# Kernel optimization log

Measured on AMD Instinct MI355X. Metric: run time of the kernel, lower is better.

## Reference

```python
import jax, jax.numpy as jnp
import numpy as np

E = 4_000_000   # number of edges
F = 16          # number of edge features
N = 100_000     # number of nodes (> F, so indices.max()+1 == N in the torch code)


def setup_inputs() -> dict:
    key = jax.random.key(0)
    k1, k2 = jax.random.split(key)
    edge_attrs = jax.random.normal(k1, (E, F), dtype=jnp.float32)
    attr_idx = jax.random.randint(k2, (2, E), 0, N, dtype=jnp.int64)
    # Pin the max node id so torch's data-dependent output size (indices.max()+1)
    # equals N deterministically.
    attr_idx = attr_idx.at[0, 0].set(N - 1)
    return {"edge_attrs": edge_attrs, "attr_idx": attr_idx, "n_nodes": N}


def reference(edge_attrs, attr_idx, n_nodes):
    # Faithful to the torch module: values are edge_attrs.view(-1) in row-major
    # order (e*F + f), but the COO indices are built in tiled order (f*E + e).
    # Hence the value summed into bucket (src[e], feature k) is
    # edge_attrs.flatten()[k*E + e]  ==  edge_attrs.reshape(-1).reshape(F, E)[k, e].
    n_edges, n_feats = edge_attrs.shape
    vals = edge_attrs.reshape(-1).reshape(n_feats, n_edges)  # (F, E)
    src = attr_idx[0]  # parent node per edge; torch.sparse.sum reduces over dst
    out = jax.ops.segment_sum(vals.T, src, num_segments=n_nodes)  # (N, F)
    return out
```

## Files before the change

### kernel.cpp

```cpp
#include <hip/hip_runtime.h>
#include <hip/hip_bf16.h>


#define F_FEATS 16
#define NPB 128
#define NB_MAX 1024
#define EPB 4096
#define TP 1024
#define RPT 4
#define TB 512
#define MAXBLK 1024
#define CAP_MAX 6144
#define RRT (CAP_MAX / TB)

__global__ __launch_bounds__(256) void mp_hist(
    const int* __restrict__ src, int* __restrict__ counts,
    int E, int nbuckets)
{
    __shared__ int s_hist[NB_MAX];
    const int tid = threadIdx.x;
    const int base = blockIdx.x * EPB;
    for (int i = tid; i < nbuckets; i += 256) s_hist[i] = 0;
    __syncthreads();
#pragma unroll
    for (int i = 0; i < 4; ++i) {
        int e = base + tid * 4 + i * 1024;
        if (e + 3 < E) {
            int4 s = *reinterpret_cast<const int4*>(src + e);
            atomicAdd(&s_hist[s.x >> 7], 1);
            atomicAdd(&s_hist[s.y >> 7], 1);
            atomicAdd(&s_hist[s.z >> 7], 1);
            atomicAdd(&s_hist[s.w >> 7], 1);
        } else {
            for (int j = 0; j < 4; ++j)
                if (e + j < E) atomicAdd(&s_hist[src[e + j] >> 7], 1);
        }
    }
    __syncthreads();
    size_t row = (size_t)blockIdx.x * nbuckets;
    for (int i = tid; i < nbuckets; i += 256) counts[row + i] = s_hist[i];
}

__global__ __launch_bounds__(256) void mp_scan(
    int* __restrict__ cnt_bases,
    int* __restrict__ totals, int nblocksA, int nbuckets)
{
    __shared__ int s[MAXBLK];
    const int b = blockIdx.x, tid = threadIdx.x;
    int orig[MAXBLK / 256];
#pragma unroll
    for (int k = 0; k < MAXBLK / 256; ++k) {
        int j = tid + k * 256;
        orig[k] = (j < nblocksA) ? cnt_bases[(size_t)j * nbuckets + b] : 0;
        s[j] = orig[k];
    }
    __syncthreads();
    for (int off = 1; off < MAXBLK; off <<= 1) {
        int v[MAXBLK / 256];
#pragma unroll
        for (int k = 0; k < MAXBLK / 256; ++k) {
            int j = tid + k * 256;
            v[k] = (j >= off) ? s[j - off] : 0;
        }
        __syncthreads();
#pragma unroll
        for (int k = 0; k < MAXBLK / 256; ++k) s[tid + k * 256] += v[k];
        __syncthreads();
    }
#pragma unroll
    for (int k = 0; k < MAXBLK / 256; ++k) {
        int j = tid + k * 256;
        if (j < nblocksA)
            cnt_bases[(size_t)j * nbuckets + b] = s[j] - orig[k];
    }
    if (tid == 0) totals[b] = s[MAXBLK - 1];
}

__global__ __launch_bounds__(TP) void mp_place_sorted(
    const float* __restrict__ vals,
    const int*   __restrict__ src,
    const int*   __restrict__ bases,
    int*         __restrict__ ids,
    float*       __restrict__ vrec,
    int E, int cap, int nbuckets)
{
    __shared__ int s_cnt[NB_MAX];
    __shared__ int s_pre[NB_MAX];
    __shared__ int s_gb[NB_MAX];
    __shared__ int s_pk[EPB];
    __shared__ int s_slot[EPB];
    __shared__ int s_tot;

    const int tid = threadIdx.x;
    const int bs  = blockIdx.x * EPB;
    const int* brow = bases + (size_t)blockIdx.x * nbuckets;

    for (int i = tid; i < NB_MAX; i += TP) s_cnt[i] = 0;
    for (int i = tid; i < nbuckets; i += TP) s_gb[i] = brow[i];
    __syncthreads();

    int n_reg[RPT];
#pragma unroll
    for (int i = 0; i < RPT; ++i) {
        int e = bs + tid + i * TP;
        n_reg[i] = (e < E) ? src[e] : -1;
    }
#pragma unroll
    for (int i = 0; i < RPT; ++i)
        if (n_reg[i] >= 0) atomicAdd(&s_cnt[n_reg[i] >> 7], 1);
    __syncthreads();

    int oc = s_cnt[tid];
    s_pre[tid] = oc;
    __syncthreads();
    for (int off = 1; off < NB_MAX; off <<= 1) {
        int v = (tid >= off) ? s_pre[tid - off] : 0;
        __syncthreads();
        s_pre[tid] += v;
        __syncthreads();
    }
    if (tid == NB_MAX - 1) s_tot = s_pre[tid];
    s_pre[tid] -= oc;
    __syncthreads();
    s_cnt[tid] = s_pre[tid];
    __syncthreads();

#pragma unroll
    for (int i = 0; i < RPT; ++i) {
        int n = n_reg[i];
        if (n < 0) continue;
        int e = bs + tid + i * TP;
        int b = n >> 7;
        int p = atomicAdd(&s_cnt[b], 1);
        s_pk[p] = (n << 12) | (e - bs);
        int r = p - s_pre[b];
        int g = s_gb[b] + r;
        s_slot[p] = (g < cap) ? (b * cap + g) : -1;
    }
    __syncthreads();

    const int total = s_tot;
    int off_r[RPT], slot_r[RPT], pk_r[RPT];
    bool val_r[RPT];
#pragma unroll
    for (int i = 0; i < RPT; ++i) {
        int p = tid + i * TP;
        val_r[i] = (p < total);
        pk_r[i]  = val_r[i] ? s_pk[p] : 0;
        slot_r[i] = val_r[i] ? s_slot[p] : -1;
        off_r[i] = pk_r[i] & 0xFFF;
    }

    float v[RPT][F_FEATS];
#pragma unroll
    for (int k = 0; k < F_FEATS; ++k) {
        const float* row = vals + (size_t)k * E + bs;
#pragma unroll
        for (int i = 0; i < RPT; ++i)
            if (val_r[i]) v[i][k] = row[off_r[i]];
    }

#pragma unroll
    for (int i = 0; i < RPT; ++i) {
        int slot = slot_r[i];
        if (slot >= 0) {
            ids[slot] = pk_r[i] >> 12;
            float4* d = reinterpret_cast<float4*>(vrec + (size_t)slot * F_FEATS);
            d[0] = make_float4(v[i][0],  v[i][1],  v[i][2],  v[i][3]);
            d[1] = make_float4(v[i][4],  v[i][5],  v[i][6],  v[i][7]);
            d[2] = make_float4(v[i][8],  v[i][9],  v[i][10], v[i][11]);
            d[3] = make_float4(v[i][12], v[i][13], v[i][14], v[i][15]);
        }
    }
}

__global__ __launch_bounds__(TB) void mp_reduce_seg(
    const int*   __restrict__ totals,
    const int*   __restrict__ ids,
    const float* __restrict__ vrec,
    float*       __restrict__ out,
    int cap, int N)
{
    __shared__ unsigned short s_perm[CAP_MAX];
    __shared__ int s_cnt[NPB];
    __shared__ int s_start[NPB + 1];
    const int b = blockIdx.x, tid = threadIdx.x;

    for (int i = tid; i < NPB; i += TB) s_cnt[i] = 0;
    __syncthreads();

    int cnt = totals[b];
    if (cnt > cap) cnt = cap;
    const size_t bkt = (size_t)b * cap;
    const int* idr = ids + bkt;

    int loc_r[RRT], rnk_r[RRT];
#pragma unroll
    for (int i = 0; i < RRT; ++i) {
        int r = tid + i * TB;
        if (r < cnt) {
            int l = idr[r] & (NPB - 1);
            loc_r[i] = l;
            rnk_r[i] = atomicAdd(&s_cnt[l], 1);
        } else {
            loc_r[i] = -1; rnk_r[i] = 0;
        }
    }
    __syncthreads();

    if (tid < NPB) s_start[tid + 1] = s_cnt[tid];
    if (tid == 0) s_start[0] = 0;
    __syncthreads();
    for (int off = 1; off < NPB; off <<= 1) {
        int v = 0;
        if (tid < NPB) {
            int j = tid + 1;
            v = (j > off) ? s_start[j - off] : 0;
        }
        __syncthreads();
        if (tid < NPB) s_start[tid + 1] += v;
        __syncthreads();
    }

#pragma unroll
    for (int i = 0; i < RRT; ++i) {
        if (loc_r[i] >= 0)
            s_perm[s_start[loc_r[i]] + rnk_r[i]] = (unsigned short)(tid + i * TB);
    }
    __syncthreads();

    const int g = tid >> 2, q = tid & 3;
    const float4* vr4 = reinterpret_cast<const float4*>(vrec) + bkt * 4;
    int j = s_start[g];
    const int j1 = s_start[g + 1];
    float4 acc = make_float4(0.f, 0.f, 0.f, 0.f);
    for (; j + 1 < j1; j += 2) {
        int r0 = s_perm[j], r1 = s_perm[j + 1];
        float4 v0 = vr4[r0 * 4 + q];
        float4 v1 = vr4[r1 * 4 + q];
        acc.x += v0.x; acc.y += v0.y; acc.z += v0.z; acc.w += v0.w;
        acc.x += v1.x; acc.y += v1.y; acc.z += v1.z; acc.w += v1.w;
    }
    if (j < j1) {
        int r0 = s_perm[j];
        float4 v0 = vr4[r0 * 4 + q];
        acc.x += v0.x; acc.y += v0.y; acc.z += v0.z; acc.w += v0.w;
    }

    int node = b * NPB + g;
    if (node < N)
        reinterpret_cast<float4*>(out)[(size_t)node * 4 + q] = acc;
}

__global__ __launch_bounds__(256) void mp_scatter_fallback(
    const float* __restrict__ vals, const int* __restrict__ src,
    float* __restrict__ out, long long E)
{
    long long e = ((long long)blockIdx.x * blockDim.x + threadIdx.x) * 4;
    if (e >= E) return;
    int4 s = *reinterpret_cast<const int4*>(src + e);
    long long b0 = (long long)s.x * F_FEATS, b1 = (long long)s.y * F_FEATS;
    long long b2 = (long long)s.z * F_FEATS, b3 = (long long)s.w * F_FEATS;
#pragma unroll
    for (int k = 0; k < F_FEATS; ++k) {
        float4 v = *reinterpret_cast<const float4*>(vals + (long long)k * E + e);
        atomicAdd(out + b0 + k, v.x);
        atomicAdd(out + b1 + k, v.y);
        atomicAdd(out + b2 + k, v.z);
        atomicAdd(out + b3 + k, v.w);
    }
}

extern "C" void kernel_launch(void* const* d_in, const int* in_sizes, int n_in,
                              void* d_out, int out_size, void* d_ws, size_t ws_size,
                              hipStream_t stream) {
    const float* edge_attrs = (const float*)d_in[0];
    const int*   attr_idx   = (const int*)d_in[1];
    int E = in_sizes[1] / 2;
    int N = out_size / F_FEATS;

    int nbuckets = (N + NPB - 1) / NPB;
    int gridA    = (E + EPB - 1) / EPB;
    long long avg = (long long)E / nbuckets;
    int cap = (int)(((avg + avg / 8 + 255) / 256) * 256);

    size_t off_tot    = 0;
    size_t off_counts = ((size_t)nbuckets * 4 + 255) & ~(size_t)255;
    size_t off_ids    = (off_counts + (size_t)gridA * nbuckets * 4 + 255) & ~(size_t)255;
    size_t off_vrec   = (off_ids    + (size_t)nbuckets * cap * 4 + 255) & ~(size_t)255;
    size_t need       = off_vrec + (size_t)nbuckets * cap * F_FEATS * 4;

    if (ws_size >= need && nbuckets <= NB_MAX && gridA <= MAXBLK && cap <= CAP_MAX) {
        int*   totals = (int*)((char*)d_ws + off_tot);
        int*   counts = (int*)((char*)d_ws + off_counts);
        int*   ids    = (int*)((char*)d_ws + off_ids);
        float* vrec   = (float*)((char*)d_ws + off_vrec);

        mp_hist<<<gridA, 256, 0, stream>>>(attr_idx, counts, E, nbuckets);
        mp_scan<<<nbuckets, 256, 0, stream>>>(counts, totals, gridA, nbuckets);
        mp_place_sorted<<<gridA, TP, 0, stream>>>(edge_attrs, attr_idx, counts,
                                                  ids, vrec, E, cap, nbuckets);
        mp_reduce_seg<<<nbuckets, TB, 0, stream>>>(totals, ids, vrec,
                                                   (float*)d_out, cap, N);
    } else {
        hipMemsetAsync(d_out, 0, (size_t)out_size * sizeof(float), stream);
        long long threads = ((long long)E + 3) / 4;
        long long grid = (threads + 255) / 256;
        mp_scatter_fallback<<<(dim3)(unsigned)grid, 256, 0, stream>>>(
            edge_attrs, attr_idx, (float*)d_out, E);
    }
}
```

Before: 654.6 us.

## Stage bucket records through LDS in chunks and use nontemporal stores in placement

The reduce kernel now walks each bucket in chunks of 1024 records. It streams each chunk's values coalesced from global memory into LDS, sorts the chunk by local node, and accumulates from LDS rather than doing scattered global float4 gathers. This removes the CAP_MAX limit on bucket capacity but adds a per-chunk scan and more barriers. The placement kernel now writes values in four phases of four features, with a block barrier between phases and nontemporal stores for both records and ids, to cut cache pollution and register pressure.

```diff
diff --git a/kernel.cpp b/kernel.cpp
--- a/kernel.cpp
+++ b/kernel.cpp
@@ -8,10 +8,11 @@
 #define EPB 4096
 #define TP 1024
 #define RPT 4
-#define TB 512
+#define TBR 512
+#define CHUNK 1024
 #define MAXBLK 1024
-#define CAP_MAX 6144
-#define RRT (CAP_MAX / TB)
+
+typedef float fvec4 __attribute__((ext_vector_type(4)));
 
 __global__ __launch_bounds__(256) void mp_hist(
     const int* __restrict__ src, int* __restrict__ counts,
@@ -151,105 +152,115 @@
         off_r[i] = pk_r[i] & 0xFFF;
     }
 
-    float v[RPT][F_FEATS];
-#pragma unroll
-    for (int k = 0; k < F_FEATS; ++k) {
-        const float* row = vals + (size_t)k * E + bs;
-#pragma unroll
-        for (int i = 0; i < RPT; ++i)
-            if (val_r[i]) v[i][k] = row[off_r[i]];
-    }
-
-#pragma unroll
-    for (int i = 0; i < RPT; ++i) {
-        int slot = slot_r[i];
-        if (slot >= 0) {
-            ids[slot] = pk_r[i] >> 12;
-            float4* d = reinterpret_cast<float4*>(vrec + (size_t)slot * F_FEATS);
-            d[0] = make_float4(v[i][0],  v[i][1],  v[i][2],  v[i][3]);
-            d[1] = make_float4(v[i][4],  v[i][5],  v[i][6],  v[i][7]);
-            d[2] = make_float4(v[i][8],  v[i][9],  v[i][10], v[i][11]);
-            d[3] = make_float4(v[i][12], v[i][13], v[i][14], v[i][15]);
-        }
-    }
-}
-
-__global__ __launch_bounds__(TB) void mp_reduce_seg(
+#pragma unroll
+    for (int ph = 0; ph < 4; ++ph) {
+        const float* r0 = vals + (size_t)(ph * 4 + 0) * E + bs;
+        const float* r1 = vals + (size_t)(ph * 4 + 1) * E + bs;
+        const float* r2 = vals + (size_t)(ph * 4 + 2) * E + bs;
+        const float* r3 = vals + (size_t)(ph * 4 + 3) * E + bs;
+        float v0[RPT], v1[RPT], v2[RPT], v3[RPT];
+#pragma unroll
+        for (int i = 0; i < RPT; ++i) {
+            if (val_r[i]) {
+                v0[i] = r0[off_r[i]]; v1[i] = r1[off_r[i]];
+                v2[i] = r2[off_r[i]]; v3[i] = r3[off_r[i]];
+            }
+        }
+#pragma unroll
+        for (int i = 0; i < RPT; ++i) {
+            if (slot_r[i] >= 0) {
+                fvec4 w = {v0[i], v1[i], v2[i], v3[i]};
+                __builtin_nontemporal_store(w,
+                    reinterpret_cast<fvec4*>(vrec + (size_t)slot_r[i] * F_FEATS) + ph);
+            }
+        }
+        __syncthreads();
+    }
+#pragma unroll
+    for (int i = 0; i < RPT; ++i)
+        if (slot_r[i] >= 0)
+            __builtin_nontemporal_store(pk_r[i] >> 12, &ids[slot_r[i]]);
+}
+
+__global__ __launch_bounds__(TBR) void mp_reduce_lds(
     const int*   __restrict__ totals,
     const int*   __restrict__ ids,
     const float* __restrict__ vrec,
     float*       __restrict__ out,
     int cap, int N)
 {
-    __shared__ unsigned short s_perm[CAP_MAX];
+    __shared__ fvec4 s_v[CHUNK * 4];
+    __shared__ unsigned short s_perm[CHUNK];
     __shared__ int s_cnt[NPB];
     __shared__ int s_start[NPB + 1];
+
     const int b = blockIdx.x, tid = threadIdx.x;
-
-    for (int i = tid; i < NPB; i += TB) s_cnt[i] = 0;
-    __syncthreads();
-
     int cnt = totals[b];
     if (cnt > cap) cnt = cap;
     const size_t bkt = (size_t)b * cap;
     const int* idr = ids + bkt;
-
-    int loc_r[RRT], rnk_r[RRT];
-#pragma unroll
-    for (int i = 0; i < RRT; ++i) {
-        int r = tid + i * TB;
-        if (r < cnt) {
-            int l = idr[r] & (NPB - 1);
-            loc_r[i] = l;
-            rnk_r[i] = atomicAdd(&s_cnt[l], 1);
-        } else {
-            loc_r[i] = -1; rnk_r[i] = 0;
-        }
-    }
-    __syncthreads();
-
-    if (tid < NPB) s_start[tid + 1] = s_cnt[tid];
-    if (tid == 0) s_start[0] = 0;
-    __syncthreads();
-    for (int off = 1; off < NPB; off <<= 1) {
-        int v = 0;
-        if (tid < NPB) {
-            int j = tid + 1;
-            v = (j > off) ? s_start[j - off] : 0;
-        }
-        __syncthreads();
-        if (tid < NPB) s_start[tid + 1] += v;
-        __syncthreads();
-    }
-
-#pragma unroll
-    for (int i = 0; i < RRT; ++i) {
-        if (loc_r[i] >= 0)
-            s_perm[s_start[loc_r[i]] + rnk_r[i]] = (unsigned short)(tid + i * TB);
-    }
-    __syncthreads();
-
+    const fvec4* vr4 = reinterpret_cast<const fvec4*>(vrec) + bkt * 4;
     const int g = tid >> 2, q = tid & 3;
-    const float4* vr4 = reinterpret_cast<const float4*>(vrec) + bkt * 4;
-    int j = s_start[g];
-    const int j1 = s_start[g + 1];
-    float4 acc = make_float4(0.f, 0.f, 0.f, 0.f);
-    for (; j + 1 < j1; j += 2) {
-        int r0 = s_perm[j], r1 = s_perm[j + 1];
-        float4 v0 = vr4[r0 * 4 + q];
-        float4 v1 = vr4[r1 * 4 + q];
-        acc.x += v0.x; acc.y += v0.y; acc.z += v0.z; acc.w += v0.w;
-        acc.x += v1.x; acc.y += v1.y; acc.z += v1.z; acc.w += v1.w;
-    }
-    if (j < j1) {
-        int r0 = s_perm[j];
-        float4 v0 = vr4[r0 * 4 + q];
-        acc.x += v0.x; acc.y += v0.y; acc.z += v0.z; acc.w += v0.w;
+    fvec4 acc = {0.f, 0.f, 0.f, 0.f};
+
+    for (int c0 = 0; c0 < cnt; c0 += CHUNK) {
+        int m = cnt - c0;
+        if (m > CHUNK) m = CHUNK;
+        const int m4 = m * 4;
+
+        fvec4 gv[8];
+#pragma unroll
+        for (int i = 0; i < 8; ++i) {
+            int j = tid + i * TBR;
+            if (j < m4)
+                gv[i] = __builtin_nontemporal_load(&vr4[(size_t)c0 * 4 + j]);
+        }
+        int e0 = tid, e1 = tid + TBR;
+        int l0 = -1, l1 = -1, r0 = 0, r1 = 0;
+        if (e0 < m) l0 = idr[c0 + e0] & (NPB - 1);
+        if (e1 < m) l1 = idr[c0 + e1] & (NPB - 1);
+
+        if (tid < NPB) s_cnt[tid] = 0;
+        __syncthreads();
+        if (l0 >= 0) r0 = atomicAdd(&s_cnt[l0], 1);
+        if (l1 >= 0) r1 = atomicAdd(&s_cnt[l1], 1);
+        __syncthreads();
+
+        if (tid < NPB) s_start[tid + 1] = s_cnt[tid];
+        if (tid == 0) s_start[0] = 0;
+        __syncthreads();
+        for (int off = 1; off < NPB; off <<= 1) {
+            int v = 0;
+            if (tid < NPB) {
+                int j = tid + 1;
+                v = (j > off) ? s_start[j - off] : 0;
+            }
+            __syncthreads();
+            if (tid < NPB) s_start[tid + 1] += v;
+            __syncthreads();
+        }
+
+        if (l0 >= 0) s_perm[s_start[l0] + r0] = (unsigned short)e0;
+        if (l1 >= 0) s_perm[s_start[l1] + r1] = (unsigned short)e1;
+#pragma unroll
+        for (int i = 0; i < 8; ++i) {
+            int j = tid + i * TBR;
+            if (j < m4) s_v[j] = gv[i];
+        }
+        __syncthreads();
+
+        const int js = s_start[g], je = s_start[g + 1];
+        for (int j = js; j < je; ++j) {
+            int rec = s_perm[j];
+            fvec4 v = s_v[rec * 4 + q];
+            acc += v;
+        }
+        __syncthreads();
     }
 
     int node = b * NPB + g;
     if (node < N)
-        reinterpret_cast<float4*>(out)[(size_t)node * 4 + q] = acc;
+        reinterpret_cast<fvec4*>(out)[(size_t)node * 4 + q] = acc;
 }
 
 __global__ __launch_bounds__(256) void mp_scatter_fallback(
@@ -290,7 +301,7 @@
     size_t off_vrec   = (off_ids    + (size_t)nbuckets * cap * 4 + 255) & ~(size_t)255;
     size_t need       = off_vrec + (size_t)nbuckets * cap * F_FEATS * 4;
 
-    if (ws_size >= need && nbuckets <= NB_MAX && gridA <= MAXBLK && cap <= CAP_MAX) {
+    if (ws_size >= need && nbuckets <= NB_MAX && gridA <= MAXBLK) {
         int*   totals = (int*)((char*)d_ws + off_tot);
         int*   counts = (int*)((char*)d_ws + off_counts);
         int*   ids    = (int*)((char*)d_ws + off_ids);
@@ -300,10 +311,10 @@
         mp_scan<<<nbuckets, 256, 0, stream>>>(counts, totals, gridA, nbuckets);
         mp_place_sorted<<<gridA, TP, 0, stream>>>(edge_attrs, attr_idx, counts,
                                                   ids, vrec, E, cap, nbuckets);
-        mp_reduce_seg<<<nbuckets, TB, 0, stream>>>(totals, ids, vrec,
-                                                   (float*)d_out, cap, N);
+        mp_reduce_lds<<<nbuckets, TBR, 0, stream>>>(totals, ids, vrec,
+                                                    (float*)d_out, cap, N);
     } else {
-        hipMemsetAsync(d_out, 0, (size_t)out_size * sizeof(float), stream);
+        (void)hipMemsetAsync(d_out, 0, (size_t)out_size * sizeof(float), stream);
         long long threads = ((long long)E + 3) / 4;
         long long grid = (threads + 255) / 256;
         mp_scatter_fallback<<<(dim3)(unsigned)grid, 256, 0, stream>>>(
```

After: 969.6 us. 48.1% more time.
